# Performance work log

Measured on AMD Instinct MI355X. Metric: run time of the kernel, lower is better.

Reference implementation:

```python
import jax, jax.numpy as jnp
import numpy as np

B, P_LEN, Q_LEN, HID = 8, 2048, 1024, 1024


def setup_inputs() -> dict:
    key = jax.random.key(0)
    k1, k2, k3, k4 = jax.random.split(key, 4)
    k = jax.random.normal(k1, (B, P_LEN, HID), dtype=jnp.float32)
    q = jax.random.normal(k2, (B, Q_LEN, HID), dtype=jnp.float32)
    # q_mask: True = pad token. All-valid mask (no pads) to avoid NaN rows.
    q_mask = jnp.zeros((B, Q_LEN), dtype=bool)
    # Xavier-normal-initialized Linear weights, shape [out, in] as in torch.
    std = float(np.sqrt(2.0 / (HID + HID)))
    Wk = jax.random.normal(k3, (HID, HID), dtype=jnp.float32) * std
    Wq = jax.random.normal(k4, (HID, HID), dtype=jnp.float32) * std
    return {"k": k, "q": q, "q_mask": q_mask, "Wk": Wk, "Wq": Wq}


def reference(k, q, q_mask, Wk, Wq):
    # relu-projected keys/queries (Linear has no bias)
    p_key = jax.nn.relu(jnp.einsum('bpd,hd->bph', k, Wk))   # [B, p_len, hid]
    q_key = jax.nn.relu(jnp.einsum('bqd,hd->bqh', q, Wq))   # [B, q_len, hid]
    scores = jnp.einsum('bph,bqh->bpq', p_key, q_key)        # [B, p_len, q_len]
    scores = jnp.where(q_mask[:, None, :], -jnp.inf, scores)
    alphas = jax.nn.softmax(scores, axis=-1)                 # [B, p_len, q_len]
    ctx = jnp.einsum('bpq,bqd->bpd', alphas, q)              # [B, p_len, q_dim]
    return ctx, alphas
```

## Files before the change

kernel.cpp:

```cpp
#include <hip/hip_runtime.h>
#include <hip/hip_bf16.h>
#include <math.h>


typedef _Float16 v8h __attribute__((ext_vector_type(8)));
typedef _Float16 v4h __attribute__((ext_vector_type(4)));
typedef float v4f __attribute__((ext_vector_type(4)));

#define AS1C(p) ((const __attribute__((address_space(1))) void*)(p))
#define AS3(p)  ((__attribute__((address_space(3))) void*)(p))

__global__ __launch_bounds__(256) void gemm_nt_f16(
    const _Float16* __restrict__ A, const _Float16* __restrict__ B,
    float* __restrict__ Cf, _Float16* __restrict__ Ch,
    int M, int N, int K,
    long long sA, long long sB, long long sC, int relu)
{
  __shared__ _Float16 As[128 * 32];
  __shared__ _Float16 Bs[128 * 32];

  const int bz = blockIdx.z;
  A += (long long)bz * sA;
  B += (long long)bz * sB;

  const int m0 = blockIdx.y * 128;
  const int n0 = blockIdx.x * 128;
  const int t  = threadIdx.x;
  const int l  = t & 63;
  const int w  = t >> 6;
  const int wm = (w >> 1) * 64;
  const int wn = (w & 1) * 64;
  const int fr = l & 15;
  const int fq = l >> 4;

  const int srow = t >> 2;
  const int scol = (t & 3) << 3;

  v4f acc[4][4];
#pragma unroll
  for (int i = 0; i < 4; ++i)
#pragma unroll
    for (int j = 0; j < 4; ++j)
      acc[i][j] = (v4f){0.f, 0.f, 0.f, 0.f};

  const _Float16* Ap = A + (long long)(m0 + srow) * K + scol;
  const _Float16* Bp = B + (long long)(n0 + srow) * K + scol;

  for (int k0 = 0; k0 < K; k0 += 32) {
    __builtin_amdgcn_global_load_lds(AS1C(Ap + k0),        AS3(As + t * 8),         16, 0, 0);
    __builtin_amdgcn_global_load_lds(AS1C(Ap + 64 * K + k0), AS3(As + 2048 + t * 8), 16, 0, 0);
    __builtin_amdgcn_global_load_lds(AS1C(Bp + k0),        AS3(Bs + t * 8),         16, 0, 0);
    __builtin_amdgcn_global_load_lds(AS1C(Bp + 64 * K + k0), AS3(Bs + 2048 + t * 8), 16, 0, 0);
    __syncthreads();

    v8h a[4], b[4];
#pragma unroll
    for (int i = 0; i < 4; ++i)
      a[i] = *(const v8h*)&As[(wm + i * 16 + fr) * 32 + fq * 8];
#pragma unroll
    for (int j = 0; j < 4; ++j)
      b[j] = *(const v8h*)&Bs[(wn + j * 16 + fr) * 32 + fq * 8];

#pragma unroll
    for (int i = 0; i < 4; ++i)
#pragma unroll
      for (int j = 0; j < 4; ++j)
        acc[i][j] = __builtin_amdgcn_mfma_f32_16x16x32_f16(a[i], b[j], acc[i][j], 0, 0, 0);

    __syncthreads();
  }

  float* Cfb = Cf ? Cf + (long long)bz * sC : nullptr;
  _Float16* Chb = Ch ? Ch + (long long)bz * sC : nullptr;
#pragma unroll
  for (int i = 0; i < 4; ++i) {
#pragma unroll
    for (int j = 0; j < 4; ++j) {
#pragma unroll
      for (int r = 0; r < 4; ++r) {
        const int row = m0 + wm + i * 16 + fq * 4 + r;
        const int col = n0 + wn + j * 16 + fr;
        float v = acc[i][j][r];
        if (relu) v = fmaxf(v, 0.f);
        if (Cfb) Cfb[(long long)row * N + col] = v;
        if (Chb) Chb[(long long)row * N + col] = (_Float16)v;
      }
    }
  }
}

__global__ __launch_bounds__(256) void f32_to_f16_kernel(
    const float* __restrict__ in, _Float16* __restrict__ out, long long n)
{
  const long long i = ((long long)blockIdx.x * 256 + threadIdx.x) * 4;
  if (i >= n) return;
  const float4 v = *(const float4*)(in + i);
  v4h o = {(_Float16)v.x, (_Float16)v.y, (_Float16)v.z, (_Float16)v.w};
  *(v4h*)(out + i) = o;
}

__global__ __launch_bounds__(256) void transpose_f16_kernel(
    const float* __restrict__ q, _Float16* __restrict__ qT, int Q, int H)
{
  __shared__ float tile[64][65];
  const float* qb = q + (long long)blockIdx.z * Q * H;
  _Float16* qTb = qT + (long long)blockIdx.z * H * Q;
  const int q0 = blockIdx.x * 64, h0 = blockIdx.y * 64;
  const int t = threadIdx.x;
  const int tr = t >> 4, tc = (t & 15) << 2;
#pragma unroll
  for (int i = 0; i < 4; ++i) {
    const float4 v = *(const float4*)(qb + (long long)(q0 + tr + i * 16) * H + h0 + tc);
    tile[tr + i * 16][tc + 0] = v.x;
    tile[tr + i * 16][tc + 1] = v.y;
    tile[tr + i * 16][tc + 2] = v.z;
    tile[tr + i * 16][tc + 3] = v.w;
  }
  __syncthreads();
#pragma unroll
  for (int i = 0; i < 4; ++i) {
    const int hl = tr + i * 16;
    const int ql = tc;
    v4h o = {(_Float16)tile[ql + 0][hl], (_Float16)tile[ql + 1][hl],
             (_Float16)tile[ql + 2][hl], (_Float16)tile[ql + 3][hl]};
    *(v4h*)(qTb + (long long)(h0 + hl) * Q + q0 + ql) = o;
  }
}

__global__ __launch_bounds__(256) void softmax_rows_kernel(
    float* __restrict__ S, _Float16* __restrict__ S16,
    const unsigned char* __restrict__ qmask, int Q, int P)
{
  const long long row = blockIdx.x;
  const int b = (int)(row / P);
  float* s = S + row * (long long)Q;
  const unsigned char* msk = qmask + (long long)b * Q;
  const int t = threadIdx.x;
  float4 v = *(const float4*)(s + (t << 2));
  float vals[4] = {v.x, v.y, v.z, v.w};
#pragma unroll
  for (int j = 0; j < 4; ++j)
    if (msk[(t << 2) + j]) vals[j] = -INFINITY;

  __shared__ float red[8];
  const int wid = t >> 6, lid = t & 63;

  float mx = fmaxf(fmaxf(vals[0], vals[1]), fmaxf(vals[2], vals[3]));
#pragma unroll
  for (int o = 32; o > 0; o >>= 1) mx = fmaxf(mx, __shfl_xor(mx, o, 64));
  if (lid == 0) red[wid] = mx;
  __syncthreads();
  mx = fmaxf(fmaxf(red[0], red[1]), fmaxf(red[2], red[3]));

  float e[4];
  float sum = 0.f;
#pragma unroll
  for (int j = 0; j < 4; ++j) { e[j] = __expf(vals[j] - mx); sum += e[j]; }
#pragma unroll
  for (int o = 32; o > 0; o >>= 1) sum += __shfl_xor(sum, o, 64);
  __syncthreads();
  if (lid == 0) red[4 + wid] = sum;
  __syncthreads();
  sum = red[4] + red[5] + red[6] + red[7];
  const float inv = 1.f / sum;

  float4 o;
  o.x = e[0] * inv; o.y = e[1] * inv; o.z = e[2] * inv; o.w = e[3] * inv;
  *(float4*)(s + (t << 2)) = o;
  v4h oh = {(_Float16)o.x, (_Float16)o.y, (_Float16)o.z, (_Float16)o.w};
  *(v4h*)(S16 + row * (long long)Q + (t << 2)) = oh;
}

extern "C" void kernel_launch(void* const* d_in, const int* in_sizes, int n_in,
                              void* d_out, int out_size, void* d_ws, size_t ws_size,
                              hipStream_t stream)
{
  const int B = 8, P = 2048, Q = 1024, H = 1024;
  const float* k  = (const float*)d_in[0];
  const float* q  = (const float*)d_in[1];
  const unsigned char* qmask = (const unsigned char*)d_in[2];
  const float* Wk = (const float*)d_in[3];
  const float* Wq = (const float*)d_in[4];

  float* ctx    = (float*)d_out;
  float* alphas = ctx + (size_t)B * P * H;

  _Float16* pkey16 = (_Float16*)d_out;

  char* wsb = (char*)d_ws;
  _Float16* qkey16   = (_Float16*)(wsb);
  _Float16* k16      = (_Float16*)(wsb + 16777216);
  _Float16* alphas16 = k16;
  _Float16* q16      = (_Float16*)(wsb + 16777216 + 33554432);
  _Float16* qT16     = q16;
  _Float16* Wk16     = (_Float16*)(wsb + 67108864);
  _Float16* Wq16     = (_Float16*)(wsb + 69206016);

  const long long nK = (long long)B * P * H;
  const long long nQ = (long long)B * Q * H;
  const long long nW = (long long)H * H;

  f32_to_f16_kernel<<<(int)(nK / 1024), 256, 0, stream>>>(k, k16, nK);
  f32_to_f16_kernel<<<(int)(nQ / 1024), 256, 0, stream>>>(q, q16, nQ);
  f32_to_f16_kernel<<<(int)(nW / 1024), 256, 0, stream>>>(Wk, Wk16, nW);
  f32_to_f16_kernel<<<(int)(nW / 1024), 256, 0, stream>>>(Wq, Wq16, nW);

  gemm_nt_f16<<<dim3(H / 128, (B * P) / 128, 1), 256, 0, stream>>>(
      k16, Wk16, nullptr, pkey16, B * P, H, H, 0LL, 0LL, 0LL, 1);
  gemm_nt_f16<<<dim3(H / 128, (B * Q) / 128, 1), 256, 0, stream>>>(
      q16, Wq16, nullptr, qkey16, B * Q, H, H, 0LL, 0LL, 0LL, 1);
  gemm_nt_f16<<<dim3(Q / 128, P / 128, B), 256, 0, stream>>>(
      pkey16, qkey16, alphas, nullptr, P, Q, H,
      (long long)P * H, (long long)Q * H, (long long)P * Q, 0);
  transpose_f16_kernel<<<dim3(Q / 64, H / 64, B), 256, 0, stream>>>(q, qT16, Q, H);
  softmax_rows_kernel<<<B * P, 256, 0, stream>>>(alphas, alphas16, qmask, Q, P);
  gemm_nt_f16<<<dim3(H / 128, P / 128, B), 256, 0, stream>>>(
      alphas16, qT16, ctx, nullptr, P, H, Q,
      (long long)P * Q, (long long)H * Q, (long long)P * H, 0);
}
```

Before: 467.9 us.

## Shrink GEMM tile to 128x64, use 1D M-fastest grid, fuse conversion kernels

The GEMM tile drops from 128x128 to 128x64 and occupancy is hinted at four blocks per CU. The grid becomes 1D with M-tiles varying fastest, so consecutive blocks share the same B tile in cache. The four f32-to-f16 conversion launches are merged into one kernel. The smaller tile doubles the block count and lowers register pressure, at the cost of more A-tile reloads and a lower MFMA-to-load ratio.

```diff
diff --git a/kernel.cpp b/kernel.cpp
--- a/kernel.cpp
+++ b/kernel.cpp
@@ -10,61 +10,64 @@
 #define AS1C(p) ((const __attribute__((address_space(1))) void*)(p))
 #define AS3(p)  ((__attribute__((address_space(3))) void*)(p))
 
-__global__ __launch_bounds__(256) void gemm_nt_f16(
+__global__ __launch_bounds__(256, 4) void gemm_nt_f16(
     const _Float16* __restrict__ A, const _Float16* __restrict__ B,
     float* __restrict__ Cf, _Float16* __restrict__ Ch,
-    int M, int N, int K,
+    int N, int K, int Mtiles, int Ntiles,
     long long sA, long long sB, long long sC, int relu)
 {
   __shared__ _Float16 As[128 * 32];
-  __shared__ _Float16 Bs[128 * 32];
-
-  const int bz = blockIdx.z;
+  __shared__ _Float16 Bs[64 * 32];
+
+  const int bid = blockIdx.x;
+  const int mt  = bid % Mtiles;
+  const int nt  = (bid / Mtiles) % Ntiles;
+  const int bz  = bid / (Mtiles * Ntiles);
+
   A += (long long)bz * sA;
   B += (long long)bz * sB;
 
-  const int m0 = blockIdx.y * 128;
-  const int n0 = blockIdx.x * 128;
+  const int m0 = mt * 128;
+  const int n0 = nt * 64;
   const int t  = threadIdx.x;
   const int l  = t & 63;
   const int w  = t >> 6;
   const int wm = (w >> 1) * 64;
-  const int wn = (w & 1) * 64;
+  const int wn = (w & 1) * 32;
   const int fr = l & 15;
   const int fq = l >> 4;
 
   const int srow = t >> 2;
   const int scol = (t & 3) << 3;
 
-  v4f acc[4][4];
+  v4f acc[4][2];
 #pragma unroll
   for (int i = 0; i < 4; ++i)
 #pragma unroll
-    for (int j = 0; j < 4; ++j)
+    for (int j = 0; j < 2; ++j)
       acc[i][j] = (v4f){0.f, 0.f, 0.f, 0.f};
 
   const _Float16* Ap = A + (long long)(m0 + srow) * K + scol;
   const _Float16* Bp = B + (long long)(n0 + srow) * K + scol;
 
   for (int k0 = 0; k0 < K; k0 += 32) {
-    __builtin_amdgcn_global_load_lds(AS1C(Ap + k0),        AS3(As + t * 8),         16, 0, 0);
+    __builtin_amdgcn_global_load_lds(AS1C(Ap + k0),          AS3(As + t * 8),        16, 0, 0);
     __builtin_amdgcn_global_load_lds(AS1C(Ap + 64 * K + k0), AS3(As + 2048 + t * 8), 16, 0, 0);
-    __builtin_amdgcn_global_load_lds(AS1C(Bp + k0),        AS3(Bs + t * 8),         16, 0, 0);
-    __builtin_amdgcn_global_load_lds(AS1C(Bp + 64 * K + k0), AS3(Bs + 2048 + t * 8), 16, 0, 0);
+    __builtin_amdgcn_global_load_lds(AS1C(Bp + k0),          AS3(Bs + t * 8),        16, 0, 0);
     __syncthreads();
 
-    v8h a[4], b[4];
+    v8h a[4], b[2];
 #pragma unroll
     for (int i = 0; i < 4; ++i)
       a[i] = *(const v8h*)&As[(wm + i * 16 + fr) * 32 + fq * 8];
 #pragma unroll
-    for (int j = 0; j < 4; ++j)
+    for (int j = 0; j < 2; ++j)
       b[j] = *(const v8h*)&Bs[(wn + j * 16 + fr) * 32 + fq * 8];
 
 #pragma unroll
     for (int i = 0; i < 4; ++i)
 #pragma unroll
-      for (int j = 0; j < 4; ++j)
+      for (int j = 0; j < 2; ++j)
         acc[i][j] = __builtin_amdgcn_mfma_f32_16x16x32_f16(a[i], b[j], acc[i][j], 0, 0, 0);
 
     __syncthreads();
@@ -75,7 +78,7 @@
 #pragma unroll
   for (int i = 0; i < 4; ++i) {
 #pragma unroll
-    for (int j = 0; j < 4; ++j) {
+    for (int j = 0; j < 2; ++j) {
 #pragma unroll
       for (int r = 0; r < 4; ++r) {
         const int row = m0 + wm + i * 16 + fq * 4 + r;
@@ -89,14 +92,23 @@
   }
 }
 
-__global__ __launch_bounds__(256) void f32_to_f16_kernel(
-    const float* __restrict__ in, _Float16* __restrict__ out, long long n)
-{
-  const long long i = ((long long)blockIdx.x * 256 + threadIdx.x) * 4;
-  if (i >= n) return;
-  const float4 v = *(const float4*)(in + i);
+__global__ __launch_bounds__(256) void convert_all_kernel(
+    const float* __restrict__ s0, _Float16* __restrict__ d0, int b0,
+    const float* __restrict__ s1, _Float16* __restrict__ d1, int b1,
+    const float* __restrict__ s2, _Float16* __restrict__ d2, int b2,
+    const float* __restrict__ s3, _Float16* __restrict__ d3)
+{
+  int blk = blockIdx.x;
+  const float* src;
+  _Float16* dst;
+  if (blk < b0)           { src = s0; dst = d0; }
+  else if (blk < b0 + b1) { src = s1; dst = d1; blk -= b0; }
+  else if (blk < b0 + b1 + b2) { src = s2; dst = d2; blk -= b0 + b1; }
+  else                    { src = s3; dst = d3; blk -= b0 + b1 + b2; }
+  const long long i = ((long long)blk * 256 + threadIdx.x) * 4;
+  const float4 v = *(const float4*)(src + i);
   v4h o = {(_Float16)v.x, (_Float16)v.y, (_Float16)v.z, (_Float16)v.w};
-  *(v4h*)(out + i) = o;
+  *(v4h*)(dst + i) = o;
 }
 
 __global__ __launch_bounds__(256) void transpose_f16_kernel(
@@ -200,21 +212,20 @@
   const long long nQ = (long long)B * Q * H;
   const long long nW = (long long)H * H;
 
-  f32_to_f16_kernel<<<(int)(nK / 1024), 256, 0, stream>>>(k, k16, nK);
-  f32_to_f16_kernel<<<(int)(nQ / 1024), 256, 0, stream>>>(q, q16, nQ);
-  f32_to_f16_kernel<<<(int)(nW / 1024), 256, 0, stream>>>(Wk, Wk16, nW);
-  f32_to_f16_kernel<<<(int)(nW / 1024), 256, 0, stream>>>(Wq, Wq16, nW);
-
-  gemm_nt_f16<<<dim3(H / 128, (B * P) / 128, 1), 256, 0, stream>>>(
-      k16, Wk16, nullptr, pkey16, B * P, H, H, 0LL, 0LL, 0LL, 1);
-  gemm_nt_f16<<<dim3(H / 128, (B * Q) / 128, 1), 256, 0, stream>>>(
-      q16, Wq16, nullptr, qkey16, B * Q, H, H, 0LL, 0LL, 0LL, 1);
-  gemm_nt_f16<<<dim3(Q / 128, P / 128, B), 256, 0, stream>>>(
-      pkey16, qkey16, alphas, nullptr, P, Q, H,
+  const int bK = (int)(nK / 1024), bQ = (int)(nQ / 1024), bW = (int)(nW / 1024);
+  convert_all_kernel<<<bK + bQ + 2 * bW, 256, 0, stream>>>(
+      k, k16, bK, q, q16, bQ, Wk, Wk16, bW, Wq, Wq16);
+
+  gemm_nt_f16<<<(16384 / 128) * (1024 / 64), 256, 0, stream>>>(
+      k16, Wk16, nullptr, pkey16, H, H, 16384 / 128, 1024 / 64, 0LL, 0LL, 0LL, 1);
+  gemm_nt_f16<<<(8192 / 128) * (1024 / 64), 256, 0, stream>>>(
+      q16, Wq16, nullptr, qkey16, H, H, 8192 / 128, 1024 / 64, 0LL, 0LL, 0LL, 1);
+  gemm_nt_f16<<<(P / 128) * (Q / 64) * B, 256, 0, stream>>>(
+      pkey16, qkey16, alphas, nullptr, Q, H, P / 128, Q / 64,
       (long long)P * H, (long long)Q * H, (long long)P * Q, 0);
   transpose_f16_kernel<<<dim3(Q / 64, H / 64, B), 256, 0, stream>>>(q, qT16, Q, H);
   softmax_rows_kernel<<<B * P, 256, 0, stream>>>(alphas, alphas16, qmask, Q, P);
-  gemm_nt_f16<<<dim3(H / 128, P / 128, B), 256, 0, stream>>>(
-      alphas16, qT16, ctx, nullptr, P, H, Q,
+  gemm_nt_f16<<<(P / 128) * (H / 64) * B, 256, 0, stream>>>(
+      alphas16, qT16, ctx, nullptr, H, Q, P / 128, H / 64,
       (long long)P * Q, (long long)H * Q, (long long)P * H, 0);
 }
```

After: 434.1 us. -7.2%, faster.
